# Performance work log

Measured on AMD Instinct MI355X. Metric: run time of the kernel, lower is better.

Reference implementation:

```python
import jax, jax.numpy as jnp
import numpy as np

NUM_EXPERTS = 8
TOP_K = 2
HIDDEN = 1024
INTER = 4096
LB_WEIGHT = 0.01


def setup_inputs() -> dict:
    key = jax.random.key(0)
    ks = jax.random.split(key, 6)
    s = 0.02
    return {
        "hidden_states": jax.random.normal(ks[0], (2, 2048, HIDDEN), dtype=jnp.float32),
        "Wg": jax.random.normal(ks[1], (HIDDEN, NUM_EXPERTS), dtype=jnp.float32) * s,
        "w1": jax.random.normal(ks[2], (NUM_EXPERTS, HIDDEN, INTER), dtype=jnp.float32) * s,
        "b1": jnp.zeros((NUM_EXPERTS, INTER), dtype=jnp.float32),
        "w2": jax.random.normal(ks[3], (NUM_EXPERTS, INTER, HIDDEN), dtype=jnp.float32) * s,
        "b2": jnp.zeros((NUM_EXPERTS, HIDDEN), dtype=jnp.float32),
    }


def reference(hidden_states, Wg, w1, b1, w2, b2):
    B, S, H = hidden_states.shape
    x = hidden_states.reshape(-1, H)            # [T, H]
    T = x.shape[0]

    # 1. Gating: softmax over experts, top-k selection, renormalized gates
    probs = jax.nn.softmax(x @ Wg, axis=-1)     # [T, E]
    top_v, top_i = jax.lax.top_k(probs, TOP_K)  # [T, K]
    gate = top_v / jnp.sum(top_v, axis=-1, keepdims=True)

    # Load-balancing aux loss: E * sum(frac_assigned * mean_prob) * weight
    frac = jnp.mean(jax.nn.one_hot(top_i, NUM_EXPERTS, dtype=probs.dtype), axis=(0, 1))  # [E]
    mean_p = jnp.mean(probs, axis=0)            # [E]
    aux_loss = NUM_EXPERTS * jnp.sum(frac * mean_p) * LB_WEIGHT

    # Combine weights: per-token weight for each expert (sum of matching top-k gates)
    combine = jnp.zeros((T, NUM_EXPERTS), dtype=x.dtype)
    combine = combine.at[jnp.arange(T)[:, None], top_i].add(gate)  # [T, E]

    # 2-4. Expert FFN + weighted combine (math-equivalent dense-per-expert form)
    out = jnp.zeros_like(x)
    for e in range(NUM_EXPERTS):
        h = jax.nn.gelu(x @ w1[e] + b1[e])       # [T, INTER]
        out = out + combine[:, e:e + 1] * (h @ w2[e] + b2[e])
    return out.reshape(B, S, H), aux_loss
```

## Files before the change

### kernel.cpp

```cpp
#include <hip/hip_runtime.h>
#include <hip/hip_bf16.h>

#define T_TOK   4096
#define HID     1024
#define INTER   4096
#define NEXP    8
#define MAXT    72
#define MAXSLOT 9216
#define TPB_TOK 16

typedef __attribute__((ext_vector_type(8))) short s16x8;
typedef __attribute__((ext_vector_type(4))) float f32x4;

__device__ __forceinline__ void load_lds16(const void* g, void* l) {
    __builtin_amdgcn_global_load_lds(
        (const __attribute__((address_space(1))) void*)g,
        (__attribute__((address_space(3))) void*)l, 16, 0, 0);
}

__device__ __forceinline__ float gelu_tanh(float v) {
    float c = 0.7978845608028654f;
    float z = c * (v + 0.044715f * v * v * v);
    return v / (1.0f + __expf(-2.0f * z));
}

__global__ void transpose_bf16_kernel(const float* __restrict__ in, __hip_bfloat16* __restrict__ out,
                                      int R, int C) {
    __shared__ float tile[64][65];
    size_t eoff = (size_t)blockIdx.z * R * C;
    int c0 = blockIdx.x * 64, r0 = blockIdx.y * 64;
    int tid = threadIdx.x;

    int lr = tid >> 4;
    int lc = (tid & 15) * 4;
    #pragma unroll
    for (int it = 0; it < 4; ++it) {
        int r = it * 16 + lr;
        float4 v = *(const float4*)(in + eoff + (size_t)(r0 + r) * C + c0 + lc);
        tile[r][lc + 0] = v.x; tile[r][lc + 1] = v.y;
        tile[r][lc + 2] = v.z; tile[r][lc + 3] = v.w;
    }
    __syncthreads();

    int oc = tid >> 3;
    int r8 = (tid & 7) * 8;
    #pragma unroll
    for (int it = 0; it < 2; ++it) {
        int c = it * 32 + oc;
        alignas(16) __hip_bfloat16 o[8];
        #pragma unroll
        for (int j = 0; j < 8; ++j) o[j] = __float2bfloat16(tile[r8 + j][c]);
        *(s16x8*)(out + eoff + (size_t)(c0 + c) * R + r0 + r8) = *(const s16x8*)o;
    }
}

__global__ void gating_kernel(const float* __restrict__ x, const float* __restrict__ Wg,
                              __hip_bfloat16* __restrict__ xb,
                              float* __restrict__ combine, int* __restrict__ counts,
                              float* __restrict__ prob_sums, int* __restrict__ idxcap) {
    __shared__ float s_ps[NEXP];
    __shared__ int   s_cnt[NEXP];
    __shared__ int   s_base[NEXP];
    __shared__ int   s_ei[TPB_TOK][2];
    __shared__ int   s_rk[TPB_TOK][2];

    int tid = threadIdx.x, wv = tid >> 6, ln = tid & 63;
    if (tid < NEXP) { s_ps[tid] = 0.f; s_cnt[tid] = 0; }
    __syncthreads();

    int t0 = blockIdx.x * TPB_TOK;
    for (int sub = 0; sub < 4; ++sub) {
        int tl = wv * 4 + sub;
        int t = t0 + tl;
        const float* xr = x + (size_t)t * HID + ln * 16;
        float4 xv[4];
        #pragma unroll
        for (int i = 0; i < 4; ++i) xv[i] = *(const float4*)(xr + i * 4);

        alignas(16) __hip_bfloat16 row[16];
        #pragma unroll
        for (int i = 0; i < 4; ++i) {
            row[i * 4 + 0] = __float2bfloat16(xv[i].x);
            row[i * 4 + 1] = __float2bfloat16(xv[i].y);
            row[i * 4 + 2] = __float2bfloat16(xv[i].z);
            row[i * 4 + 3] = __float2bfloat16(xv[i].w);
        }
        __hip_bfloat16* xbr = xb + (size_t)t * HID + ln * 16;
        *(s16x8*)(xbr)     = *(s16x8*)&row[0];
        *(s16x8*)(xbr + 8) = *(s16x8*)&row[8];

        float acc[NEXP] = {0,0,0,0,0,0,0,0};
        #pragma unroll
        for (int i = 0; i < 4; ++i) {
            float xs[4] = {xv[i].x, xv[i].y, xv[i].z, xv[i].w};
            #pragma unroll
            for (int j = 0; j < 4; ++j) {
                int k = ln * 16 + i * 4 + j;
                float4 wa = *(const float4*)(Wg + (size_t)k * 8);
                float4 wb = *(const float4*)(Wg + (size_t)k * 8 + 4);
                acc[0] += xs[j] * wa.x; acc[1] += xs[j] * wa.y;
                acc[2] += xs[j] * wa.z; acc[3] += xs[j] * wa.w;
                acc[4] += xs[j] * wb.x; acc[5] += xs[j] * wb.y;
                acc[6] += xs[j] * wb.z; acc[7] += xs[j] * wb.w;
            }
        }
        #pragma unroll
        for (int e = 0; e < NEXP; ++e)
            #pragma unroll
            for (int off = 32; off >= 1; off >>= 1)
                acc[e] += __shfl_xor(acc[e], off);

        float m = acc[0];
        #pragma unroll
        for (int e = 1; e < NEXP; ++e) m = fmaxf(m, acc[e]);
        float p[NEXP], s = 0.f;
        #pragma unroll
        for (int e = 0; e < NEXP; ++e) { p[e] = __expf(acc[e] - m); s += p[e]; }
        float inv = 1.0f / s;
        #pragma unroll
        for (int e = 0; e < NEXP; ++e) p[e] *= inv;

        int i0 = 0;
        #pragma unroll
        for (int e = 1; e < NEXP; ++e) if (p[e] > p[i0]) i0 = e;
        int i1 = (i0 == 0) ? 1 : 0;
        #pragma unroll
        for (int e = 0; e < NEXP; ++e) if (e != i0 && p[e] > p[i1]) i1 = e;
        float gs = p[i0] + p[i1];
        float g0 = p[i0] / gs, g1 = p[i1] / gs;

        if (ln == 0) {
            float rowc[NEXP] = {0,0,0,0,0,0,0,0};
            rowc[i0] = g0; rowc[i1] = g1;
            float4* cr = (float4*)(combine + (size_t)t * NEXP);
            cr[0] = make_float4(rowc[0], rowc[1], rowc[2], rowc[3]);
            cr[1] = make_float4(rowc[4], rowc[5], rowc[6], rowc[7]);
            #pragma unroll
            for (int e = 0; e < NEXP; ++e) atomicAdd(&s_ps[e], p[e]);
            int r0 = atomicAdd(&s_cnt[i0], 1);
            int r1 = atomicAdd(&s_cnt[i1], 1);
            s_ei[tl][0] = i0; s_rk[tl][0] = r0;
            s_ei[tl][1] = i1; s_rk[tl][1] = r1;
        }
    }
    __syncthreads();
    if (tid < NEXP) {
        s_base[tid] = atomicAdd(&counts[tid], s_cnt[tid]);
        atomicAdd(&prob_sums[tid], s_ps[tid]);
    }
    __syncthreads();
    if (tid < TPB_TOK * 2) {
        int tl = tid >> 1, k = tid & 1;
        int e = s_ei[tl][k];
        idxcap[e * T_TOK + s_base[e] + s_rk[tl][k]] = t0 + tl;
    }
}

__global__ void plan_kernel(const int* __restrict__ counts, const float* __restrict__ prob_sums,
                            int* __restrict__ offs, int* __restrict__ tile_e,
                            int* __restrict__ tile_s0, int* __restrict__ tile_nv,
                            int* __restrict__ ntiles, float* __restrict__ aux_out) {
    int tt = 0, o = 0;
    for (int e = 0; e < NEXP; ++e) {
        offs[e] = o;
        int n = counts[e];
        int nt = (n + 127) >> 7;
        for (int r = 0; r < nt; ++r) {
            tile_e[tt] = e;
            tile_s0[tt] = o + r * 128;
            int nv = n - r * 128; if (nv > 128) nv = 128;
            tile_nv[tt] = nv;
            ++tt;
        }
        o += nt * 128;
    }
    *ntiles = tt;
    float aux = 0.f;
    for (int e = 0; e < NEXP; ++e)
        aux += ((float)counts[e] / (float)(T_TOK * 2)) * (prob_sums[e] / (float)T_TOK);
    aux_out[0] = (float)NEXP * aux * 0.01f;
}

__global__ void compact_kernel(const int* __restrict__ counts, const int* __restrict__ offs,
                               const int* __restrict__ tile_e, const int* __restrict__ tile_s0,
                               const int* __restrict__ ntiles,
                               const int* __restrict__ idxcap, int* __restrict__ idxc) {
    int tt = blockIdx.x;
    if (tt >= *ntiles) return;
    int e = tile_e[tt];
    int slot = tile_s0[tt] + threadIdx.x;
    int i = slot - offs[e];
    int n = counts[e];
    idxc[slot] = (i < n) ? idxcap[e * T_TOK + i] : 0;
}


__global__ __launch_bounds__(256, 3)
void gemm1_kernel(const __hip_bfloat16* __restrict__ xb,
                  const __hip_bfloat16* __restrict__ w1b,
                  const float* __restrict__ b1,
                  const int* __restrict__ idxc,
                  const int* __restrict__ tile_e, const int* __restrict__ tile_s0,
                  const int* __restrict__ ntiles,
                  __hip_bfloat16* __restrict__ h)
{
    const int NWG = MAXT * (INTER / 128);
    int bid = blockIdx.x;
    int w = (bid & 7) * (NWG / 8) + (bid >> 3);
    int tt = w >> 5;
    int n0 = (w & 31) * 128;
    if (tt >= *ntiles) return;
    int e = tile_e[tt];
    int slot0 = tile_s0[tt];

    __shared__ __hip_bfloat16 As[2][128][32];
    __shared__ __hip_bfloat16 Bs[2][128][32];
    __shared__ int s_idx[128];

    int tid = threadIdx.x, wv = tid >> 6, ln = tid & 63;
    if (tid < 128) s_idx[tid] = idxc[slot0 + tid];
    __syncthreads();

    int sg = ((ln & 3) ^ ((ln >> 3) & 3)) * 8;
    unsigned offA[2], offB[2];
    #pragma unroll
    for (int j = 0; j < 2; ++j) {
        int r = wv * 32 + j * 16 + (ln >> 2);
        offA[j] = (unsigned)(s_idx[r] * HID + sg);
        offB[j] = (unsigned)(((unsigned)(e * INTER + n0 + r)) * HID + sg);
    }

    f32x4 acc[4][4] = {};
    int wr = wv >> 1, wc = wv & 1, lr = ln & 15;
    int pA = ((ln >> 4) ^ ((lr >> 1) & 3)) * 16;

    auto STAGE = [&](int b, int kt) {
        #pragma unroll
        for (int j = 0; j < 2; ++j) {
            load_lds16(xb  + offA[j] + kt, (void*)&As[b][wv * 32 + j * 16][0]);
            load_lds16(w1b + offB[j] + kt, (void*)&Bs[b][wv * 32 + j * 16][0]);
        }
    };
    auto COMPUTE = [&](int b) {
        s16x8 af[4], bf[4];
        #pragma unroll
        for (int m = 0; m < 4; ++m) {
            int row = wr * 64 + m * 16 + lr;
            af[m] = *(const s16x8*)((const char*)&As[b][0][0] + row * 64 + pA);
        }
        #pragma unroll
        for (int n = 0; n < 4; ++n) {
            int row = wc * 64 + n * 16 + lr;
            bf[n] = *(const s16x8*)((const char*)&Bs[b][0][0] + row * 64 + pA);
        }
        #pragma unroll
        for (int m = 0; m < 4; ++m)
            #pragma unroll
            for (int n = 0; n < 4; ++n)
                acc[m][n] = __builtin_amdgcn_mfma_f32_16x16x32_bf16(af[m], bf[n], acc[m][n], 0, 0, 0);
    };

    STAGE(0, 0);
    __syncthreads();
    const int NT = HID / 32;
    for (int t = 0; t < NT - 1; ++t) {
        STAGE((t + 1) & 1, (t + 1) * 32);
        COMPUTE(t & 1);
        __syncthreads();
    }
    COMPUTE((NT - 1) & 1);

    const float* b1e = b1 + (size_t)e * INTER;
    int rq = (ln >> 4) * 4;
    #pragma unroll
    for (int m = 0; m < 4; ++m) {
        #pragma unroll
        for (int r = 0; r < 4; ++r) {
            int row = wr * 64 + m * 16 + rq + r;
            size_t hrow = (size_t)(slot0 + row) * INTER;
            #pragma unroll
            for (int n = 0; n < 4; ++n) {
                int col = n0 + wc * 64 + n * 16 + lr;
                float v = acc[m][n][r] + b1e[col];
                h[hrow + col] = __float2bfloat16(gelu_tanh(v));
            }
        }
    }
}

__global__ __launch_bounds__(256, 3)
void gemm2_kernel(const __hip_bfloat16* __restrict__ h,
                  const __hip_bfloat16* __restrict__ w2b,
                  const float* __restrict__ b2,
                  const float* __restrict__ combine,
                  const int* __restrict__ idxc,
                  const int* __restrict__ tile_e, const int* __restrict__ tile_s0,
                  const int* __restrict__ tile_nv, const int* __restrict__ ntiles,
                  float* __restrict__ out)
{
    const int NWG = MAXT * (HID / 128) * 2;
    int bid = blockIdx.x;
    int w = (bid & 7) * (NWG / 8) + (bid >> 3);
    int ks = w & 1;
    int n0 = ((w >> 1) & 7) * 128;
    int tt = w >> 4;
    if (tt >= *ntiles) return;
    int e = tile_e[tt];
    int slot0 = tile_s0[tt];

    __shared__ __hip_bfloat16 As[2][128][32];
    __shared__ __hip_bfloat16 Bs[2][128][32];
    __shared__ int s_idx[128];

    int tid = threadIdx.x, wv = tid >> 6, ln = tid & 63;
    if (tid < 128) s_idx[tid] = idxc[slot0 + tid];
    __syncthreads();

    int sg = ((ln & 3) ^ ((ln >> 3) & 3)) * 8;
    unsigned offA[2], offB[2];
    #pragma unroll
    for (int j = 0; j < 2; ++j) {
        int r = wv * 32 + j * 16 + (ln >> 2);
        offA[j] = (unsigned)((unsigned)(slot0 + r) * INTER + sg);
        offB[j] = (unsigned)(((unsigned)(e * HID + n0 + r)) * INTER + sg);
    }

    f32x4 acc[4][4] = {};
    int wr = wv >> 1, wc = wv & 1, lr = ln & 15;
    int pA = ((ln >> 4) ^ ((lr >> 1) & 3)) * 16;

    auto STAGE = [&](int b, int kt) {
        #pragma unroll
        for (int j = 0; j < 2; ++j) {
            load_lds16(h   + offA[j] + kt, (void*)&As[b][wv * 32 + j * 16][0]);
            load_lds16(w2b + offB[j] + kt, (void*)&Bs[b][wv * 32 + j * 16][0]);
        }
    };
    auto COMPUTE = [&](int b) {
        s16x8 af[4], bf[4];
        #pragma unroll
        for (int m = 0; m < 4; ++m) {
            int row = wr * 64 + m * 16 + lr;
            af[m] = *(const s16x8*)((const char*)&As[b][0][0] + row * 64 + pA);
        }
        #pragma unroll
        for (int n = 0; n < 4; ++n) {
            int row = wc * 64 + n * 16 + lr;
            bf[n] = *(const s16x8*)((const char*)&Bs[b][0][0] + row * 64 + pA);
        }
        #pragma unroll
        for (int m = 0; m < 4; ++m)
            #pragma unroll
            for (int n = 0; n < 4; ++n)
                acc[m][n] = __builtin_amdgcn_mfma_f32_16x16x32_bf16(af[m], bf[n], acc[m][n], 0, 0, 0);
    };

    int k0 = ks * (INTER / 2);
    STAGE(0, k0);
    __syncthreads();
    const int NT = (INTER / 2) / 32;
    for (int t = 0; t < NT - 1; ++t) {
        STAGE((t + 1) & 1, k0 + (t + 1) * 32);
        COMPUTE(t & 1);
        __syncthreads();
    }
    COMPUTE((NT - 1) & 1);

    const float* b2e = b2 + (size_t)e * HID;
    int nv = tile_nv[tt];
    int rq = (ln >> 4) * 4;
    #pragma unroll
    for (int m = 0; m < 4; ++m) {
        #pragma unroll
        for (int r = 0; r < 4; ++r) {
            int row = wr * 64 + m * 16 + rq + r;
            if (row < nv) {
                int tok = s_idx[row];
                float g = combine[(size_t)tok * 8 + e];
                #pragma unroll
                for (int n = 0; n < 4; ++n) {
                    int col = n0 + wc * 64 + n * 16 + lr;
                    float v = acc[m][n][r] + (ks == 0 ? b2e[col] : 0.f);
                    atomicAdd(&out[(size_t)tok * HID + col], g * v);
                }
            }
        }
    }
}

static const size_t OFF_XB      = 0;
static const size_t SZ_XB       = (size_t)T_TOK * HID * 2;
static const size_t OFF_W1B     = OFF_XB + SZ_XB;
static const size_t SZ_W        = (size_t)NEXP * INTER * HID * 2;
static const size_t OFF_W2B     = OFF_W1B + SZ_W;
static const size_t OFF_H       = OFF_W2B + SZ_W;
static const size_t SZ_H        = (size_t)MAXSLOT * INTER * 2;
static const size_t OFF_COMBINE = OFF_H + SZ_H;
static const size_t OFF_IDXCAP  = OFF_COMBINE + (size_t)T_TOK * 8 * 4;
static const size_t OFF_IDXC    = OFF_IDXCAP + (size_t)NEXP * T_TOK * 4;
static const size_t OFF_COUNTS  = OFF_IDXC + (size_t)MAXSLOT * 4;
static const size_t OFF_PSUMS   = OFF_COUNTS + 32;
static const size_t OFF_OFFS    = OFF_PSUMS + 32;
static const size_t OFF_TILE_E  = OFF_OFFS + 64;
static const size_t OFF_TILE_S0 = OFF_TILE_E + 512;
static const size_t OFF_TILE_NV = OFF_TILE_S0 + 512;
static const size_t OFF_NTILES  = OFF_TILE_NV + 512;

extern "C" void kernel_launch(void* const* d_in, const int* in_sizes, int n_in,
                              void* d_out, int out_size, void* d_ws, size_t ws_size,
                              hipStream_t stream) {
    const float* x  = (const float*)d_in[0];
    const float* Wg = (const float*)d_in[1];
    const float* w1 = (const float*)d_in[2];
    const float* b1 = (const float*)d_in[3];
    const float* w2 = (const float*)d_in[4];
    const float* b2 = (const float*)d_in[5];
    float* out = (float*)d_out;
    char* ws = (char*)d_ws;

    __hip_bfloat16* xb   = (__hip_bfloat16*)(ws + OFF_XB);
    __hip_bfloat16* w1b  = (__hip_bfloat16*)(ws + OFF_W1B);
    __hip_bfloat16* w2b  = (__hip_bfloat16*)(ws + OFF_W2B);
    __hip_bfloat16* h    = (__hip_bfloat16*)(ws + OFF_H);
    float* combine       = (float*)(ws + OFF_COMBINE);
    int*   idxcap        = (int*)(ws + OFF_IDXCAP);
    int*   idxc          = (int*)(ws + OFF_IDXC);
    int*   counts        = (int*)(ws + OFF_COUNTS);
    float* psums         = (float*)(ws + OFF_PSUMS);
    int*   offs          = (int*)(ws + OFF_OFFS);
    int*   tile_e        = (int*)(ws + OFF_TILE_E);
    int*   tile_s0       = (int*)(ws + OFF_TILE_S0);
    int*   tile_nv       = (int*)(ws + OFF_TILE_NV);
    int*   ntiles        = (int*)(ws + OFF_NTILES);

    (void)hipMemsetAsync(out, 0, (size_t)out_size * sizeof(float), stream);
    (void)hipMemsetAsync(ws + OFF_COUNTS, 0, 64, stream);

    transpose_bf16_kernel<<<dim3(INTER / 64, HID / 64, NEXP), 256, 0, stream>>>(w1, w1b, HID, INTER);
    transpose_bf16_kernel<<<dim3(HID / 64, INTER / 64, NEXP), 256, 0, stream>>>(w2, w2b, INTER, HID);
    gating_kernel<<<T_TOK / TPB_TOK, 256, 0, stream>>>(x, Wg, xb, combine, counts, psums, idxcap);
    plan_kernel<<<1, 1, 0, stream>>>(counts, psums, offs, tile_e, tile_s0, tile_nv, ntiles,
                                     out + (size_t)T_TOK * HID);
    compact_kernel<<<MAXT, 128, 0, stream>>>(counts, offs, tile_e, tile_s0, ntiles, idxcap, idxc);
    gemm1_kernel<<<MAXT * (INTER / 128), 256, 0, stream>>>(xb, w1b, b1, idxc, tile_e, tile_s0,
                                                           ntiles, h);
    gemm2_kernel<<<MAXT * (HID / 128) * 2, 256, 0, stream>>>(h, w2b, b2, combine, idxc, tile_e,
                                                             tile_s0, tile_nv, ntiles, out);
}
```

Baseline: 402.6 us.

## Enlarge MoE GEMM tiles to 256x256x64 with 512 threads and deeper prefetch

Both expert GEMMs move from 128x128 tiles with K-step 32 on 256 threads to 256x256 tiles with K-step 64 on 512 threads (8 waves, each computing 128x64). Routing plan, padding and slot capacity now work in 256-row tiles. The main loop prefetches two stages ahead, using raw s_barrier plus explicit vmcnt waits instead of __syncthreads. This is meant to raise arithmetic intensity and cut global traffic per FLOP. The cost is more padding waste per expert, fewer workgroups, about 128KB of LDS per block, and higher register pressure.

```diff
diff --git a/kernel.cpp b/kernel.cpp
--- a/kernel.cpp
+++ b/kernel.cpp
@@ -5,8 +5,8 @@
 #define HID     1024
 #define INTER   4096
 #define NEXP    8
-#define MAXT    72
-#define MAXSLOT 9216
+#define MAXT256 40
+#define MSLOT   10240
 #define TPB_TOK 16
 
 typedef __attribute__((ext_vector_type(8))) short s16x8;
@@ -164,15 +164,15 @@
     for (int e = 0; e < NEXP; ++e) {
         offs[e] = o;
         int n = counts[e];
-        int nt = (n + 127) >> 7;
+        int nt = (n + 255) >> 8;
         for (int r = 0; r < nt; ++r) {
             tile_e[tt] = e;
-            tile_s0[tt] = o + r * 128;
-            int nv = n - r * 128; if (nv > 128) nv = 128;
+            tile_s0[tt] = o + r * 256;
+            int nv = n - r * 256; if (nv > 256) nv = 256;
             tile_nv[tt] = nv;
             ++tt;
         }
-        o += nt * 128;
+        o += nt * 256;
     }
     *ntiles = tt;
     float aux = 0.f;
@@ -195,7 +195,10 @@
 }
 
 
-__global__ __launch_bounds__(256, 3)
+#define VMCNT8() asm volatile("s_waitcnt vmcnt(8)" ::: "memory")
+#define VMCNT0() asm volatile("s_waitcnt vmcnt(0)" ::: "memory")
+
+__global__ __launch_bounds__(512, 2)
 void gemm1_kernel(const __hip_bfloat16* __restrict__ xb,
                   const __hip_bfloat16* __restrict__ w1b,
                   const float* __restrict__ b1,
@@ -204,79 +207,91 @@
                   const int* __restrict__ ntiles,
                   __hip_bfloat16* __restrict__ h)
 {
-    const int NWG = MAXT * (INTER / 128);
+    const int NWG = MAXT256 * (INTER / 256);
     int bid = blockIdx.x;
     int w = (bid & 7) * (NWG / 8) + (bid >> 3);
-    int tt = w >> 5;
-    int n0 = (w & 31) * 128;
+    int tt = w >> 4;
+    int n0 = (w & 15) * 256;
     if (tt >= *ntiles) return;
     int e = tile_e[tt];
     int slot0 = tile_s0[tt];
 
-    __shared__ __hip_bfloat16 As[2][128][32];
-    __shared__ __hip_bfloat16 Bs[2][128][32];
-    __shared__ int s_idx[128];
-
-    int tid = threadIdx.x, wv = tid >> 6, ln = tid & 63;
-    if (tid < 128) s_idx[tid] = idxc[slot0 + tid];
-    __syncthreads();
-
-    int sg = ((ln & 3) ^ ((ln >> 3) & 3)) * 8;
-    unsigned offA[2], offB[2];
-    #pragma unroll
-    for (int j = 0; j < 2; ++j) {
-        int r = wv * 32 + j * 16 + (ln >> 2);
-        offA[j] = (unsigned)(s_idx[r] * HID + sg);
-        offB[j] = (unsigned)(((unsigned)(e * INTER + n0 + r)) * HID + sg);
-    }
-
-    f32x4 acc[4][4] = {};
-    int wr = wv >> 1, wc = wv & 1, lr = ln & 15;
-    int pA = ((ln >> 4) ^ ((lr >> 1) & 3)) * 16;
+    __shared__ __hip_bfloat16 As[2][256][64];
+    __shared__ __hip_bfloat16 Bs[2][256][64];
+    __shared__ int s_idx[256];
+
+    int tid = threadIdx.x, wid = tid >> 6, ln = tid & 63;
+    if (tid < 256) s_idx[tid] = idxc[slot0 + tid];
+    __syncthreads();
+
+    int ss = ((ln & 7) ^ ((ln >> 3) & 7)) * 8;
+    unsigned offA[4], offB[4];
+    #pragma unroll
+    for (int j = 0; j < 4; ++j) {
+        int r = j * 64 + wid * 8 + (ln >> 3);
+        offA[j] = (unsigned)(s_idx[r] * HID) + ss;
+        offB[j] = (unsigned)((e * INTER + n0 + r) * HID) + ss;
+    }
+
+    f32x4 acc[8][4] = {};
+    int wr = wid >> 2, wc = wid & 3, lr = ln & 15;
 
     auto STAGE = [&](int b, int kt) {
         #pragma unroll
-        for (int j = 0; j < 2; ++j) {
-            load_lds16(xb  + offA[j] + kt, (void*)&As[b][wv * 32 + j * 16][0]);
-            load_lds16(w1b + offB[j] + kt, (void*)&Bs[b][wv * 32 + j * 16][0]);
-        }
+        for (int j = 0; j < 4; ++j)
+            load_lds16(xb + offA[j] + kt, (void*)&As[b][j * 64 + wid * 8][0]);
+        #pragma unroll
+        for (int j = 0; j < 4; ++j)
+            load_lds16(w1b + offB[j] + kt, (void*)&Bs[b][j * 64 + wid * 8][0]);
     };
     auto COMPUTE = [&](int b) {
-        s16x8 af[4], bf[4];
-        #pragma unroll
-        for (int m = 0; m < 4; ++m) {
-            int row = wr * 64 + m * 16 + lr;
-            af[m] = *(const s16x8*)((const char*)&As[b][0][0] + row * 64 + pA);
-        }
-        #pragma unroll
-        for (int n = 0; n < 4; ++n) {
-            int row = wc * 64 + n * 16 + lr;
-            bf[n] = *(const s16x8*)((const char*)&Bs[b][0][0] + row * 64 + pA);
-        }
-        #pragma unroll
-        for (int m = 0; m < 4; ++m)
-            #pragma unroll
-            for (int n = 0; n < 4; ++n)
-                acc[m][n] = __builtin_amdgcn_mfma_f32_16x16x32_bf16(af[m], bf[n], acc[m][n], 0, 0, 0);
+        #pragma unroll
+        for (int ks = 0; ks < 2; ++ks) {
+            int phys = ((ks * 4 + (ln >> 4)) ^ (ln & 7)) * 16;
+            s16x8 af[8], bf[4];
+            #pragma unroll
+            for (int m = 0; m < 8; ++m) {
+                int row = wr * 128 + m * 16 + lr;
+                af[m] = *(const s16x8*)((const char*)&As[b][0][0] + row * 128 + phys);
+            }
+            #pragma unroll
+            for (int n = 0; n < 4; ++n) {
+                int row = wc * 64 + n * 16 + lr;
+                bf[n] = *(const s16x8*)((const char*)&Bs[b][0][0] + row * 128 + phys);
+            }
+            #pragma unroll
+            for (int m = 0; m < 8; ++m)
+                #pragma unroll
+                for (int n = 0; n < 4; ++n)
+                    acc[m][n] = __builtin_amdgcn_mfma_f32_16x16x32_bf16(af[m], bf[n], acc[m][n], 0, 0, 0);
+        }
     };
 
     STAGE(0, 0);
-    __syncthreads();
-    const int NT = HID / 32;
-    for (int t = 0; t < NT - 1; ++t) {
-        STAGE((t + 1) & 1, (t + 1) * 32);
+    STAGE(1, 64);
+    VMCNT8();
+    __builtin_amdgcn_s_barrier();
+
+    const int NKT = HID / 64;
+    for (int t = 0; t < NKT; ++t) {
         COMPUTE(t & 1);
-        __syncthreads();
-    }
-    COMPUTE((NT - 1) & 1);
+        __builtin_amdgcn_s_barrier();
+        if (t + 2 < NKT) {
+            STAGE(t & 1, (t + 2) * 64);
+            VMCNT8();
+        } else {
+            VMCNT0();
+        }
+        __builtin_amdgcn_s_barrier();
+    }
 
     const float* b1e = b1 + (size_t)e * INTER;
     int rq = (ln >> 4) * 4;
     #pragma unroll
-    for (int m = 0; m < 4; ++m) {
+    for (int m = 0; m < 8; ++m) {
         #pragma unroll
         for (int r = 0; r < 4; ++r) {
-            int row = wr * 64 + m * 16 + rq + r;
+            int row = wr * 128 + m * 16 + rq + r;
             size_t hrow = (size_t)(slot0 + row) * INTER;
             #pragma unroll
             for (int n = 0; n < 4; ++n) {
@@ -288,7 +303,7 @@
     }
 }
 
-__global__ __launch_bounds__(256, 3)
+__global__ __launch_bounds__(512, 2)
 void gemm2_kernel(const __hip_bfloat16* __restrict__ h,
                   const __hip_bfloat16* __restrict__ w2b,
                   const float* __restrict__ b2,
@@ -298,82 +313,94 @@
                   const int* __restrict__ tile_nv, const int* __restrict__ ntiles,
                   float* __restrict__ out)
 {
-    const int NWG = MAXT * (HID / 128) * 2;
+    const int NWG = MAXT256 * (HID / 256) * 2;
     int bid = blockIdx.x;
     int w = (bid & 7) * (NWG / 8) + (bid >> 3);
     int ks = w & 1;
-    int n0 = ((w >> 1) & 7) * 128;
-    int tt = w >> 4;
+    int n0 = ((w >> 1) & 3) * 256;
+    int tt = w >> 3;
     if (tt >= *ntiles) return;
     int e = tile_e[tt];
     int slot0 = tile_s0[tt];
 
-    __shared__ __hip_bfloat16 As[2][128][32];
-    __shared__ __hip_bfloat16 Bs[2][128][32];
-    __shared__ int s_idx[128];
-
-    int tid = threadIdx.x, wv = tid >> 6, ln = tid & 63;
-    if (tid < 128) s_idx[tid] = idxc[slot0 + tid];
-    __syncthreads();
-
-    int sg = ((ln & 3) ^ ((ln >> 3) & 3)) * 8;
-    unsigned offA[2], offB[2];
-    #pragma unroll
-    for (int j = 0; j < 2; ++j) {
-        int r = wv * 32 + j * 16 + (ln >> 2);
-        offA[j] = (unsigned)((unsigned)(slot0 + r) * INTER + sg);
-        offB[j] = (unsigned)(((unsigned)(e * HID + n0 + r)) * INTER + sg);
-    }
-
-    f32x4 acc[4][4] = {};
-    int wr = wv >> 1, wc = wv & 1, lr = ln & 15;
-    int pA = ((ln >> 4) ^ ((lr >> 1) & 3)) * 16;
+    __shared__ __hip_bfloat16 As[2][256][64];
+    __shared__ __hip_bfloat16 Bs[2][256][64];
+    __shared__ int s_idx[256];
+
+    int tid = threadIdx.x, wid = tid >> 6, ln = tid & 63;
+    if (tid < 256) s_idx[tid] = idxc[slot0 + tid];
+    __syncthreads();
+
+    int ss = ((ln & 7) ^ ((ln >> 3) & 7)) * 8;
+    unsigned offA[4], offB[4];
+    #pragma unroll
+    for (int j = 0; j < 4; ++j) {
+        int r = j * 64 + wid * 8 + (ln >> 3);
+        offA[j] = (unsigned)((slot0 + r) * INTER) + ss;
+        offB[j] = (unsigned)((e * HID + n0 + r) * INTER) + ss;
+    }
+
+    f32x4 acc[8][4] = {};
+    int wr = wid >> 2, wc = wid & 3, lr = ln & 15;
 
     auto STAGE = [&](int b, int kt) {
         #pragma unroll
-        for (int j = 0; j < 2; ++j) {
-            load_lds16(h   + offA[j] + kt, (void*)&As[b][wv * 32 + j * 16][0]);
-            load_lds16(w2b + offB[j] + kt, (void*)&Bs[b][wv * 32 + j * 16][0]);
-        }
+        for (int j = 0; j < 4; ++j)
+            load_lds16(h + offA[j] + kt, (void*)&As[b][j * 64 + wid * 8][0]);
+        #pragma unroll
+        for (int j = 0; j < 4; ++j)
+            load_lds16(w2b + offB[j] + kt, (void*)&Bs[b][j * 64 + wid * 8][0]);
     };
     auto COMPUTE = [&](int b) {
-        s16x8 af[4], bf[4];
-        #pragma unroll
-        for (int m = 0; m < 4; ++m) {
-            int row = wr * 64 + m * 16 + lr;
-            af[m] = *(const s16x8*)((const char*)&As[b][0][0] + row * 64 + pA);
-        }
-        #pragma unroll
-        for (int n = 0; n < 4; ++n) {
-            int row = wc * 64 + n * 16 + lr;
-            bf[n] = *(const s16x8*)((const char*)&Bs[b][0][0] + row * 64 + pA);
-        }
-        #pragma unroll
-        for (int m = 0; m < 4; ++m)
-            #pragma unroll
-            for (int n = 0; n < 4; ++n)
-                acc[m][n] = __builtin_amdgcn_mfma_f32_16x16x32_bf16(af[m], bf[n], acc[m][n], 0, 0, 0);
+        #pragma unroll
+        for (int ks2 = 0; ks2 < 2; ++ks2) {
+            int phys = ((ks2 * 4 + (ln >> 4)) ^ (ln & 7)) * 16;
+            s16x8 af[8], bf[4];
+            #pragma unroll
+            for (int m = 0; m < 8; ++m) {
+                int row = wr * 128 + m * 16 + lr;
+                af[m] = *(const s16x8*)((const char*)&As[b][0][0] + row * 128 + phys);
+            }
+            #pragma unroll
+            for (int n = 0; n < 4; ++n) {
+                int row = wc * 64 + n * 16 + lr;
+                bf[n] = *(const s16x8*)((const char*)&Bs[b][0][0] + row * 128 + phys);
+            }
+            #pragma unroll
+            for (int m = 0; m < 8; ++m)
+                #pragma unroll
+                for (int n = 0; n < 4; ++n)
+                    acc[m][n] = __builtin_amdgcn_mfma_f32_16x16x32_bf16(af[m], bf[n], acc[m][n], 0, 0, 0);
+        }
     };
 
     int k0 = ks * (INTER / 2);
     STAGE(0, k0);
-    __syncthreads();
-    const int NT = (INTER / 2) / 32;
-    for (int t = 0; t < NT - 1; ++t) {
-        STAGE((t + 1) & 1, k0 + (t + 1) * 32);
+    STAGE(1, k0 + 64);
+    VMCNT8();
+    __builtin_amdgcn_s_barrier();
+
+    const int NKT = (INTER / 2) / 64;
+    for (int t = 0; t < NKT; ++t) {
         COMPUTE(t & 1);
-        __syncthreads();
-    }
-    COMPUTE((NT - 1) & 1);
+        __builtin_amdgcn_s_barrier();
+        if (t + 2 < NKT) {
+            STAGE(t & 1, k0 + (t + 2) * 64);
+            VMCNT8();
+        } else {
+            VMCNT0();
+        }
+        __builtin_amdgcn_s_barrier();
+    }
 
     const float* b2e = b2 + (size_t)e * HID;
     int nv = tile_nv[tt];
     int rq = (ln >> 4) * 4;
     #pragma unroll
-    for (int m = 0; m < 4; ++m) {
+    for (int m = 0; m < 8; ++m) {
         #pragma unroll
         for (int r = 0; r < 4; ++r) {
-            int row = wr * 64 + m * 16 + rq + r;
+            int row = wr * 128 + m * 16 + rq + r;
             if (row < nv) {
                 int tok = s_idx[row];
                 float g = combine[(size_t)tok * 8 + e];
@@ -394,11 +421,11 @@
 static const size_t SZ_W        = (size_t)NEXP * INTER * HID * 2;
 static const size_t OFF_W2B     = OFF_W1B + SZ_W;
 static const size_t OFF_H       = OFF_W2B + SZ_W;
-static const size_t SZ_H        = (size_t)MAXSLOT * INTER * 2;
+static const size_t SZ_H        = (size_t)MSLOT * INTER * 2;
 static const size_t OFF_COMBINE = OFF_H + SZ_H;
 static const size_t OFF_IDXCAP  = OFF_COMBINE + (size_t)T_TOK * 8 * 4;
 static const size_t OFF_IDXC    = OFF_IDXCAP + (size_t)NEXP * T_TOK * 4;
-static const size_t OFF_COUNTS  = OFF_IDXC + (size_t)MAXSLOT * 4;
+static const size_t OFF_COUNTS  = OFF_IDXC + (size_t)MSLOT * 4;
 static const size_t OFF_PSUMS   = OFF_COUNTS + 32;
 static const size_t OFF_OFFS    = OFF_PSUMS + 32;
 static const size_t OFF_TILE_E  = OFF_OFFS + 64;
@@ -424,7 +451,7 @@
     __hip_bfloat16* h    = (__hip_bfloat16*)(ws + OFF_H);
     float* combine       = (float*)(ws + OFF_COMBINE);
     int*   idxcap        = (int*)(ws + OFF_IDXCAP);
-    int*   idxc          = (int*)(ws + OFF_IDXC);
+    int*   idxc         = (int*)(ws + OFF_IDXC);
     int*   counts        = (int*)(ws + OFF_COUNTS);
     float* psums         = (float*)(ws + OFF_PSUMS);
     int*   offs          = (int*)(ws + OFF_OFFS);
@@ -441,9 +468,9 @@
     gating_kernel<<<T_TOK / TPB_TOK, 256, 0, stream>>>(x, Wg, xb, combine, counts, psums, idxcap);
     plan_kernel<<<1, 1, 0, stream>>>(counts, psums, offs, tile_e, tile_s0, tile_nv, ntiles,
                                      out + (size_t)T_TOK * HID);
-    compact_kernel<<<MAXT, 128, 0, stream>>>(counts, offs, tile_e, tile_s0, ntiles, idxcap, idxc);
-    gemm1_kernel<<<MAXT * (INTER / 128), 256, 0, stream>>>(xb, w1b, b1, idxc, tile_e, tile_s0,
-                                                           ntiles, h);
-    gemm2_kernel<<<MAXT * (HID / 128) * 2, 256, 0, stream>>>(h, w2b, b2, combine, idxc, tile_e,
-                                                             tile_s0, tile_nv, ntiles, out);
-}
+    compact_kernel<<<MAXT256, 256, 0, stream>>>(counts, offs, tile_e, tile_s0, ntiles, idxcap, idxc);
+    gemm1_kernel<<<MAXT256 * (INTER / 256), 512, 0, stream>>>(xb, w1b, b1, idxc, tile_e, tile_s0,
+                                                              ntiles, h);
+    gemm2_kernel<<<MAXT256 * (HID / 256) * 2, 512, 0, stream>>>(h, w2b, b2, combine, idxc, tile_e,
+                                                                tile_s0, tile_nv, ntiles, out);
+}
```

After: 491.0 us. 1.22x slower.
